# Performance work log

Hardware: AMD Instinct MI355X
Metric: run time of the kernel (lower is better)

## Reference

```python
import jax, jax.numpy as jnp
import numpy as np

EMBED = 1024
HEADS = 16
HEAD_DIM = EMBED // HEADS


def setup_inputs() -> dict:
    key = jax.random.key(0)
    k1, k2, k3, k4, k5 = jax.random.split(key, 5)
    B, S, E = 4, 2048, EMBED
    scale = 1.0 / np.sqrt(E)
    return {
        "tensor": jax.random.normal(k1, (B, S, E), dtype=jnp.float32),
        "in_proj_w": jax.random.normal(k2, (3 * E, E), dtype=jnp.float32) * scale,
        "in_proj_b": jax.random.normal(k3, (3 * E,), dtype=jnp.float32) * 0.02,
        "out_proj_w": jax.random.normal(k4, (E, E), dtype=jnp.float32) * scale,
        "out_proj_b": jax.random.normal(k5, (E,), dtype=jnp.float32) * 0.02,
        "causal_mask": 1,
    }


def reference(tensor, in_proj_w, in_proj_b, out_proj_w, out_proj_b, causal_mask):
    B, S, E = tensor.shape
    H, D = HEADS, HEAD_DIM
    # fused qkv projection (torch Linear: x @ W.T + b)
    qkv = tensor @ in_proj_w.T + in_proj_b  # [B, S, 3E]
    q, k, v = jnp.split(qkv, 3, axis=-1)
    # [B, S, E] -> [B, H, S, D]
    q = q.reshape(B, S, H, D).transpose(0, 2, 1, 3)
    k = k.reshape(B, S, H, D).transpose(0, 2, 1, 3)
    v = v.reshape(B, S, H, D).transpose(0, 2, 1, 3)
    scores = jnp.einsum("bhqd,bhkd->bhqk", q, k)  # [B, H, S, S]
    if causal_mask:
        mask = jnp.triu(jnp.ones((S, S), dtype=bool), k=1)
        scores = jnp.where(mask, -jnp.inf, scores)
    scores = scores / np.sqrt(D).astype(np.float32)
    attn = jax.nn.softmax(scores, axis=-1)
    out = jnp.einsum("bhqk,bhkd->bhqd", attn, v)  # [B, H, S, D]
    out = out.transpose(0, 2, 1, 3).reshape(B, S, E)
    return out @ out_proj_w.T + out_proj_b
```

## Files before the change

### kernel.cpp

```cpp
#include <hip/hip_runtime.h>
#include <hip/hip_bf16.h>

#define B_  4
#define S_  2048
#define E_  1024
#define H_  16
#define D_  64
#define M_  (B_*S_)
#define N3_ (3*E_)

typedef __bf16 bf16;
typedef bf16  bf16x4 __attribute__((ext_vector_type(4)));
typedef bf16  bf16x8 __attribute__((ext_vector_type(8)));
typedef float f32x4  __attribute__((ext_vector_type(4)));

#define SC2 0.18033688011112043f

__device__ __forceinline__ f32x4 mfma16(bf16x8 a, bf16x8 b, f32x4 c) {
    return __builtin_amdgcn_mfma_f32_16x16x32_bf16(a, b, c, 0, 0, 0);
}

typedef const __attribute__((address_space(1))) void* gas_t;
typedef __attribute__((address_space(3))) void* las_t;
__device__ __forceinline__ void gl_lds16(const void* g, void* l) {
    __builtin_amdgcn_global_load_lds((gas_t)g, (las_t)l, 16, 0, 0);
}

#define WAITCNT_VM4() __builtin_amdgcn_s_waitcnt(0x0F74)
#define WAITCNT_VM2() __builtin_amdgcn_s_waitcnt(0x0F72)
#define WAITCNT_VM0() __builtin_amdgcn_s_waitcnt(0x0F70)

__global__ __launch_bounds__(256) void cvt_all(const float* __restrict__ x,
                                               const float* __restrict__ w_in,
                                               const float* __restrict__ w_out,
                                               bf16* __restrict__ Xbf,
                                               bf16* __restrict__ Wqkv,
                                               bf16* __restrict__ Wo) {
    const int n1 = M_ * E_ / 4, n2 = N3_ * E_ / 4, n3 = E_ * E_ / 4;
    int i = blockIdx.x * blockDim.x + threadIdx.x;
    const float* src; bf16* dst; int j;
    if (i < n1)           { src = x;     dst = Xbf;  j = i; }
    else if (i < n1 + n2) { src = w_in;  dst = Wqkv; j = i - n1; }
    else if (i < n1 + n2 + n3) { src = w_out; dst = Wo; j = i - n1 - n2; }
    else return;
    float4 v = *(const float4*)(src + (size_t)j * 4);
    bf16x4 o;
    o[0] = (bf16)v.x; o[1] = (bf16)v.y; o[2] = (bf16)v.z; o[3] = (bf16)v.w;
    *(bf16x4*)(dst + (size_t)j * 4) = o;
}

__global__ __launch_bounds__(256) void gemm_qkv(const bf16* __restrict__ X,
                                                const bf16* __restrict__ W,
                                                const float* __restrict__ bias,
                                                bf16* __restrict__ QKV,
                                                bf16* __restrict__ Vt) {
    __shared__ __align__(16) bf16 As[128 * 64];
    __shared__ __align__(16) bf16 Bs[128 * 64];
    const int t = threadIdx.x;
    const int wav = t >> 6, lane = t & 63, quad = lane >> 4, l15 = lane & 15;
    const int m0 = blockIdx.y * 128, n0 = blockIdx.x * 128;
    const int wr = (wav >> 1) * 64, wc = (wav & 1) * 64;
    const int srow = t >> 3;
    const int swz  = ((t & 7) ^ (srow & 7)) * 8;
    const bool isV = (n0 >= 2 * E_);

    const bf16* Ablk = X + (size_t)m0 * E_;
    const bf16* Bblk = W + (size_t)n0 * E_;
    f32x4 acc[4][4] = {};

    for (int kk = 0; kk < E_; kk += 64) {
        __syncthreads();
        #pragma unroll
        for (int ps = 0; ps < 4; ++ps) {
            gl_lds16(Ablk + (size_t)(srow + ps * 32) * E_ + kk + swz, As + (size_t)(t + ps * 256) * 8);
            gl_lds16(Bblk + (size_t)(srow + ps * 32) * E_ + kk + swz, Bs + (size_t)(t + ps * 256) * 8);
        }
        __syncthreads();
        #pragma unroll
        for (int ks = 0; ks < 2; ++ks) {
            bf16x8 af[4], bw[4];
            #pragma unroll
            for (int i = 0; i < 4; ++i) {
                const int ra = wr + i * 16 + l15;
                const int rb = wc + i * 16 + l15;
                const int cx = ((ks * 4 + quad) ^ (l15 & 7)) * 8;
                af[i] = *(const bf16x8*)&As[ra * 64 + cx];
                bw[i] = *(const bf16x8*)&Bs[rb * 64 + cx];
            }
            if (!isV) {
                #pragma unroll
                for (int i = 0; i < 4; ++i)
                    #pragma unroll
                    for (int j = 0; j < 4; ++j)
                        acc[i][j] = mfma16(af[i], bw[j], acc[i][j]);
            } else {
                #pragma unroll
                for (int i = 0; i < 4; ++i)
                    #pragma unroll
                    for (int j = 0; j < 4; ++j)
                        acc[i][j] = mfma16(bw[i], af[j], acc[i][j]);
            }
        }
    }
    if (!isV) {
        #pragma unroll
        for (int i = 0; i < 4; ++i)
            #pragma unroll
            for (int j = 0; j < 4; ++j)
                #pragma unroll
                for (int r = 0; r < 4; ++r) {
                    int mg = m0 + wr + i * 16 + quad * 4 + r;
                    int ng = n0 + wc + j * 16 + l15;
                    float v = acc[i][j][r] + bias[ng];
                    int which = ng >> 10, rem = ng & 1023;
                    if (which == 0) v *= SC2;
                    int h = rem >> 6, d = rem & 63;
                    int b = mg >> 11, s = mg & 2047;
                    QKV[(size_t)which * (B_ * H_ * S_ * D_) +
                        (((size_t)(b * H_ + h) * S_ + s) * D_ + d)] = (bf16)v;
                }
    } else {
        #pragma unroll
        for (int i = 0; i < 4; ++i)
            #pragma unroll
            for (int j = 0; j < 4; ++j)
                #pragma unroll
                for (int r = 0; r < 4; ++r) {
                    int ng = n0 + wc + i * 16 + quad * 4 + r;
                    int mg = m0 + wr + j * 16 + l15;
                    float v = acc[i][j][r] + bias[ng];
                    int rem = ng & 1023;
                    int h = rem >> 6, d = rem & 63;
                    int b = mg >> 11, s = mg & 2047;
                    Vt[(((size_t)(b * H_ + h) * D_ + d) * S_) + s] = (bf16)v;
                }
    }
}

__global__ __launch_bounds__(512, 4) void attn8(const bf16* __restrict__ Q,
                                                const bf16* __restrict__ K,
                                                const bf16* __restrict__ Vt,
                                                bf16* __restrict__ O) {
    __shared__ __align__(16) bf16 Ks[2][64 * 64];
    __shared__ __align__(16) bf16 Vs[2][64 * 64];
    __shared__ __align__(16) bf16 Ps[8][16 * 64];

    const int t = threadIdx.x;
    const int wav = t >> 6, lane = t & 63, quad = lane >> 4, l15 = lane & 15;
    const int p  = blockIdx.x >> 6;
    const int bh = blockIdx.x & 63;

    const bf16* Qb = Q  + (size_t)bh * S_ * D_;
    const bf16* Kb = K  + (size_t)bh * S_ * D_;
    const bf16* Vb = Vt + (size_t)bh * (size_t)D_ * S_;

    const int srow = t >> 3;
    const int swz  = ((t & 7) ^ (srow & 7)) * 8;
    bf16* Pw = &Ps[wav][0];
    const int pswz = l15 & 7;

    const int b = bh >> 4, h = bh & 15;

    #pragma unroll 1
    for (int phase = 0; phase < 2; ++phase) {
        const int qb  = phase ? (15 - p) : p;
        const int q0w = qb * 128 + wav * 16;
        const int qg  = q0w + l15;
        const int niter = 2 * qb + 2;

        __builtin_amdgcn_s_barrier();
        gl_lds16(Kb + (size_t)srow * D_ + swz, &Ks[0][(size_t)t * 8]);
        gl_lds16(Vb + (size_t)srow * S_ + swz, &Vs[0][(size_t)t * 8]);

        bf16x8 qf0 = *(const bf16x8*)&Qb[(size_t)(q0w + l15) * D_ + quad * 8];
        bf16x8 qf1 = *(const bf16x8*)&Qb[(size_t)(q0w + l15) * D_ + 32 + quad * 8];

        f32x4 oacc[4] = {};
        f32x4 psum = {0.f, 0.f, 0.f, 0.f};

        #pragma unroll 1
        for (int it = 0; it < niter; ++it) {
            const int key0 = it * 64;
            const int cur = it & 1;
            const bf16* Kc = &Ks[cur][0];
            const bf16* Vc = &Vs[cur][0];

            __builtin_amdgcn_s_barrier();
            if (it + 1 < niter) {
                const int kn = key0 + 64;
                gl_lds16(Kb + (size_t)(kn + srow) * D_ + swz, &Ks[1 - cur][(size_t)t * 8]);
                gl_lds16(Vb + (size_t)srow * S_ + kn + swz,   &Vs[1 - cur][(size_t)t * 8]);
                WAITCNT_VM2();
            } else {
                WAITCNT_VM0();
            }
            __builtin_amdgcn_s_barrier();

            f32x4 sacc[4];
            #pragma unroll
            for (int mt = 0; mt < 4; ++mt) {
                const int krow = mt * 16 + l15;
                const int sw = krow & 7;
                bf16x8 kf0 = *(const bf16x8*)&Kc[krow * 64 + ((quad ^ sw) * 8)];
                bf16x8 kf1 = *(const bf16x8*)&Kc[krow * 64 + (((4 + quad) ^ sw) * 8)];
                f32x4 a = {};
                a = mfma16(kf0, qf0, a);
                a = mfma16(kf1, qf1, a);
                sacc[mt] = a;
            }

            #pragma unroll
            for (int mt = 0; mt < 4; ++mt) {
                if (key0 + mt * 16 + 15 > q0w) {
                    #pragma unroll
                    for (int r = 0; r < 4; ++r) {
                        int key = key0 + mt * 16 + quad * 4 + r;
                        sacc[mt][r] = (key > qg) ? -3e38f : sacc[mt][r];
                    }
                }
            }

            #pragma unroll
            for (int mt = 0; mt < 4; ++mt) {
                bf16x4 pk;
                #pragma unroll
                for (int r = 0; r < 4; ++r) {
                    float pv = __builtin_amdgcn_exp2f(sacc[mt][r]);
                    psum[r] += pv;
                    pk[r] = (bf16)pv;
                }
                const int pc = ((mt * 2 + (quad >> 1)) ^ pswz) * 8 + (quad & 1) * 4;
                *(bf16x4*)&Pw[l15 * 64 + pc] = pk;
            }

            bf16x8 pf0 = *(const bf16x8*)&Pw[l15 * 64 + ((quad ^ pswz) * 8)];
            bf16x8 pf1 = *(const bf16x8*)&Pw[l15 * 64 + (((4 + quad) ^ pswz) * 8)];
            #pragma unroll
            for (int nt = 0; nt < 4; ++nt) {
                const int vrow = nt * 16 + l15;
                const int sw = vrow & 7;
                bf16x8 vf0 = *(const bf16x8*)&Vc[vrow * 64 + ((quad ^ sw) * 8)];
                bf16x8 vf1 = *(const bf16x8*)&Vc[vrow * 64 + (((4 + quad) ^ sw) * 8)];
                oacc[nt] = mfma16(pf0, vf0, oacc[nt]);
                oacc[nt] = mfma16(pf1, vf1, oacc[nt]);
            }
        }

        float rsum = psum[0] + psum[1] + psum[2] + psum[3];
        rsum += __shfl_xor(rsum, 16);
        rsum += __shfl_xor(rsum, 32);
        const float linv = 1.0f / rsum;

        #pragma unroll
        for (int rr = 0; rr < 4; ++rr) {
            float li = __shfl(linv, quad * 4 + rr);
            const int q = q0w + quad * 4 + rr;
            #pragma unroll
            for (int nt = 0; nt < 4; ++nt)
                O[((size_t)b * S_ + q) * E_ + h * D_ + nt * 16 + l15] =
                    (bf16)(oacc[nt][rr] * li);
        }
    }
}

__global__ __launch_bounds__(256) void gemm_out(const bf16* __restrict__ A,
                                                const bf16* __restrict__ W,
                                                const float* __restrict__ bias,
                                                float* __restrict__ out) {
    __shared__ __align__(16) bf16 As[128 * 64];
    __shared__ __align__(16) bf16 Bs[128 * 64];
    const int t = threadIdx.x;
    const int wav = t >> 6, lane = t & 63, quad = lane >> 4, l15 = lane & 15;
    const int m0 = blockIdx.y * 128, n0 = blockIdx.x * 128;
    const int wr = (wav >> 1) * 64, wc = (wav & 1) * 64;
    const int srow = t >> 3;
    const int swz  = ((t & 7) ^ (srow & 7)) * 8;

    const bf16* Ablk = A + (size_t)m0 * E_;
    const bf16* Bblk = W + (size_t)n0 * E_;
    f32x4 acc[4][4] = {};

    for (int kk = 0; kk < E_; kk += 64) {
        __syncthreads();
        #pragma unroll
        for (int ps = 0; ps < 4; ++ps) {
            gl_lds16(Ablk + (size_t)(srow + ps * 32) * E_ + kk + swz, As + (size_t)(t + ps * 256) * 8);
            gl_lds16(Bblk + (size_t)(srow + ps * 32) * E_ + kk + swz, Bs + (size_t)(t + ps * 256) * 8);
        }
        __syncthreads();
        #pragma unroll
        for (int ks = 0; ks < 2; ++ks) {
            bf16x8 af[4], bw[4];
            #pragma unroll
            for (int i = 0; i < 4; ++i) {
                const int ra = wr + i * 16 + l15;
                const int rb = wc + i * 16 + l15;
                const int cx = ((ks * 4 + quad) ^ (l15 & 7)) * 8;
                af[i] = *(const bf16x8*)&As[ra * 64 + cx];
                bw[i] = *(const bf16x8*)&Bs[rb * 64 + cx];
            }
            #pragma unroll
            for (int i = 0; i < 4; ++i)
                #pragma unroll
                for (int j = 0; j < 4; ++j)
                    acc[i][j] = mfma16(af[i], bw[j], acc[i][j]);
        }
    }
    #pragma unroll
    for (int i = 0; i < 4; ++i)
        #pragma unroll
        for (int j = 0; j < 4; ++j)
            #pragma unroll
            for (int r = 0; r < 4; ++r) {
                int mg = m0 + wr + i * 16 + quad * 4 + r;
                int ng = n0 + wc + j * 16 + l15;
                out[(size_t)mg * E_ + ng] = acc[i][j][r] + bias[ng];
            }
}

extern "C" void kernel_launch(void* const* d_in, const int* in_sizes, int n_in,
                              void* d_out, int out_size, void* d_ws, size_t ws_size,
                              hipStream_t stream) {
    const float* x     = (const float*)d_in[0];
    const float* w_in  = (const float*)d_in[1];
    const float* b_in  = (const float*)d_in[2];
    const float* w_out = (const float*)d_in[3];
    const float* b_out = (const float*)d_in[4];
    float* out = (float*)d_out;

    char* ws = (char*)d_ws;
    bf16* Xbf  = (bf16*)ws; ws += (size_t)M_ * E_ * 2;
    bf16* Wqkv = (bf16*)ws; ws += (size_t)N3_ * E_ * 2;
    bf16* Wo   = (bf16*)ws; ws += (size_t)E_ * E_ * 2;
    bf16* QKV  = (bf16*)ws; ws += (size_t)2 * B_ * H_ * S_ * D_ * 2;
    bf16* Vt   = (bf16*)ws; ws += (size_t)B_ * H_ * S_ * D_ * 2;
    bf16* Obf  = Xbf;

    const int nCvt = (M_ * E_ + N3_ * E_ + E_ * E_) / 4;
    cvt_all<<<(nCvt + 255) / 256, 256, 0, stream>>>(x, w_in, w_out, Xbf, Wqkv, Wo);

    gemm_qkv<<<dim3(N3_ / 128, M_ / 128), 256, 0, stream>>>(Xbf, Wqkv, b_in, QKV, Vt);

    bf16* Qp = QKV;
    bf16* Kp = QKV + (size_t)B_ * H_ * S_ * D_;

    attn8<<<dim3(8 * B_ * H_), 512, 0, stream>>>(Qp, Kp, Vt, Obf);

    gemm_out<<<dim3(E_ / 128, M_ / 128), 256, 0, stream>>>(Obf, Wo, b_out, out);
}
```

Before: 233.5 us.

## Double attention key/value tile size to 128 keys per iteration

The attention kernel now stages 128 keys of K and V per LDS buffer instead of 64, halving the loop iterations and barrier pairs per query block. Inside each iteration it processes two 64-key sub-tiles and skips the second when it lies fully above the causal diagonal. V uses a 128-wide row with a 16-way XOR swizzle. LDS use grows from about 48 KB to about 80 KB per block, which may lower the number of resident blocks per CU. The wasted masked work on the diagonal tile also grows.

```diff
diff --git a/kernel.cpp b/kernel.cpp
--- a/kernel.cpp
+++ b/kernel.cpp
@@ -27,7 +27,6 @@
 }
 
 #define WAITCNT_VM4() __builtin_amdgcn_s_waitcnt(0x0F74)
-#define WAITCNT_VM2() __builtin_amdgcn_s_waitcnt(0x0F72)
 #define WAITCNT_VM0() __builtin_amdgcn_s_waitcnt(0x0F70)
 
 __global__ __launch_bounds__(256) void cvt_all(const float* __restrict__ x,
@@ -137,12 +136,12 @@
     }
 }
 
-__global__ __launch_bounds__(512, 4) void attn8(const bf16* __restrict__ Q,
+__global__ __launch_bounds__(512, 4) void attn9(const bf16* __restrict__ Q,
                                                 const bf16* __restrict__ K,
                                                 const bf16* __restrict__ Vt,
                                                 bf16* __restrict__ O) {
-    __shared__ __align__(16) bf16 Ks[2][64 * 64];
-    __shared__ __align__(16) bf16 Vs[2][64 * 64];
+    __shared__ __align__(16) bf16 Ks[2][128 * 64];
+    __shared__ __align__(16) bf16 Vs[2][64 * 128];
     __shared__ __align__(16) bf16 Ps[8][16 * 64];
 
     const int t = threadIdx.x;
@@ -156,6 +155,9 @@
 
     const int srow = t >> 3;
     const int swz  = ((t & 7) ^ (srow & 7)) * 8;
+    const int vrow_st = t >> 4;
+    const int vswz = ((t & 15) ^ (vrow_st & 15)) * 8;
+
     bf16* Pw = &Ps[wav][0];
     const int pswz = l15 & 7;
 
@@ -166,11 +168,13 @@
         const int qb  = phase ? (15 - p) : p;
         const int q0w = qb * 128 + wav * 16;
         const int qg  = q0w + l15;
-        const int niter = 2 * qb + 2;
+        const int niter = qb + 1;
 
         __builtin_amdgcn_s_barrier();
-        gl_lds16(Kb + (size_t)srow * D_ + swz, &Ks[0][(size_t)t * 8]);
-        gl_lds16(Vb + (size_t)srow * S_ + swz, &Vs[0][(size_t)t * 8]);
+        gl_lds16(Kb + (size_t)srow * D_ + swz,            &Ks[0][(size_t)t * 8]);
+        gl_lds16(Kb + (size_t)(srow + 64) * D_ + swz,     &Ks[0][(size_t)(t + 512) * 8]);
+        gl_lds16(Vb + (size_t)vrow_st * S_ + vswz,        &Vs[0][(size_t)t * 8]);
+        gl_lds16(Vb + (size_t)(vrow_st + 32) * S_ + vswz, &Vs[0][(size_t)(t + 512) * 8]);
 
         bf16x8 qf0 = *(const bf16x8*)&Qb[(size_t)(q0w + l15) * D_ + quad * 8];
         bf16x8 qf1 = *(const bf16x8*)&Qb[(size_t)(q0w + l15) * D_ + 32 + quad * 8];
@@ -180,69 +184,79 @@
 
         #pragma unroll 1
         for (int it = 0; it < niter; ++it) {
-            const int key0 = it * 64;
+            const int key0 = it * 128;
             const int cur = it & 1;
             const bf16* Kc = &Ks[cur][0];
             const bf16* Vc = &Vs[cur][0];
 
             __builtin_amdgcn_s_barrier();
             if (it + 1 < niter) {
-                const int kn = key0 + 64;
-                gl_lds16(Kb + (size_t)(kn + srow) * D_ + swz, &Ks[1 - cur][(size_t)t * 8]);
-                gl_lds16(Vb + (size_t)srow * S_ + kn + swz,   &Vs[1 - cur][(size_t)t * 8]);
-                WAITCNT_VM2();
+                const int kn = key0 + 128;
+                bf16* Kn = &Ks[1 - cur][0];
+                bf16* Vn = &Vs[1 - cur][0];
+                gl_lds16(Kb + (size_t)(kn + srow) * D_ + swz,        Kn + (size_t)t * 8);
+                gl_lds16(Kb + (size_t)(kn + srow + 64) * D_ + swz,   Kn + (size_t)(t + 512) * 8);
+                gl_lds16(Vb + (size_t)vrow_st * S_ + kn + vswz,        Vn + (size_t)t * 8);
+                gl_lds16(Vb + (size_t)(vrow_st + 32) * S_ + kn + vswz, Vn + (size_t)(t + 512) * 8);
+                WAITCNT_VM4();
             } else {
                 WAITCNT_VM0();
             }
             __builtin_amdgcn_s_barrier();
 
-            f32x4 sacc[4];
-            #pragma unroll
-            for (int mt = 0; mt < 4; ++mt) {
-                const int krow = mt * 16 + l15;
-                const int sw = krow & 7;
-                bf16x8 kf0 = *(const bf16x8*)&Kc[krow * 64 + ((quad ^ sw) * 8)];
-                bf16x8 kf1 = *(const bf16x8*)&Kc[krow * 64 + (((4 + quad) ^ sw) * 8)];
-                f32x4 a = {};
-                a = mfma16(kf0, qf0, a);
-                a = mfma16(kf1, qf1, a);
-                sacc[mt] = a;
-            }
-
-            #pragma unroll
-            for (int mt = 0; mt < 4; ++mt) {
-                if (key0 + mt * 16 + 15 > q0w) {
+            #pragma unroll
+            for (int sub = 0; sub < 2; ++sub) {
+                const int key0s = key0 + sub * 64;
+                if (sub == 1 && q0w + 15 < key0s) continue;
+
+                f32x4 sacc[4];
+                #pragma unroll
+                for (int mt = 0; mt < 4; ++mt) {
+                    const int krow = sub * 64 + mt * 16 + l15;
+                    const int sw = krow & 7;
+                    bf16x8 kf0 = *(const bf16x8*)&Kc[krow * 64 + ((quad ^ sw) * 8)];
+                    bf16x8 kf1 = *(const bf16x8*)&Kc[krow * 64 + (((4 + quad) ^ sw) * 8)];
+                    f32x4 a = {};
+                    a = mfma16(kf0, qf0, a);
+                    a = mfma16(kf1, qf1, a);
+                    sacc[mt] = a;
+                }
+
+                #pragma unroll
+                for (int mt = 0; mt < 4; ++mt) {
+                    if (key0s + mt * 16 + 15 > q0w) {
+                        #pragma unroll
+                        for (int r = 0; r < 4; ++r) {
+                            int key = key0s + mt * 16 + quad * 4 + r;
+                            sacc[mt][r] = (key > qg) ? -3e38f : sacc[mt][r];
+                        }
+                    }
+                }
+
+                #pragma unroll
+                for (int mt = 0; mt < 4; ++mt) {
+                    bf16x4 pk;
                     #pragma unroll
                     for (int r = 0; r < 4; ++r) {
-                        int key = key0 + mt * 16 + quad * 4 + r;
-                        sacc[mt][r] = (key > qg) ? -3e38f : sacc[mt][r];
+                        float pv = __builtin_amdgcn_exp2f(sacc[mt][r]);
+                        psum[r] += pv;
+                        pk[r] = (bf16)pv;
                     }
-                }
-            }
-
-            #pragma unroll
-            for (int mt = 0; mt < 4; ++mt) {
-                bf16x4 pk;
-                #pragma unroll
-                for (int r = 0; r < 4; ++r) {
-                    float pv = __builtin_amdgcn_exp2f(sacc[mt][r]);
-                    psum[r] += pv;
-                    pk[r] = (bf16)pv;
-                }
-                const int pc = ((mt * 2 + (quad >> 1)) ^ pswz) * 8 + (quad & 1) * 4;
-                *(bf16x4*)&Pw[l15 * 64 + pc] = pk;
-            }
-
-            bf16x8 pf0 = *(const bf16x8*)&Pw[l15 * 64 + ((quad ^ pswz) * 8)];
-            bf16x8 pf1 = *(const bf16x8*)&Pw[l15 * 64 + (((4 + quad) ^ pswz) * 8)];
-            #pragma unroll
-            for (int nt = 0; nt < 4; ++nt) {
-                const int vrow = nt * 16 + l15;
-                const int sw = vrow & 7;
-                bf16x8 vf0 = *(const bf16x8*)&Vc[vrow * 64 + ((quad ^ sw) * 8)];
-                bf16x8 vf1 = *(const bf16x8*)&Vc[vrow * 64 + (((4 + quad) ^ sw) * 8)];
-                oacc[nt] = mfma16(pf0, vf0, oacc[nt]);
-                oacc[nt] = mfma16(pf1, vf1, oacc[nt]);
+                    const int pc = ((mt * 2 + (quad >> 1)) ^ pswz) * 8 + (quad & 1) * 4;
+                    *(bf16x4*)&Pw[l15 * 64 + pc] = pk;
+                }
+
+                bf16x8 pf0 = *(const bf16x8*)&Pw[l15 * 64 + ((quad ^ pswz) * 8)];
+                bf16x8 pf1 = *(const bf16x8*)&Pw[l15 * 64 + (((4 + quad) ^ pswz) * 8)];
+                #pragma unroll
+                for (int nt = 0; nt < 4; ++nt) {
+                    const int vrow = nt * 16 + l15;
+                    const int sw16 = vrow & 15;
+                    bf16x8 vf0 = *(const bf16x8*)&Vc[vrow * 128 + (((sub * 8 + quad) ^ sw16) * 8)];
+                    bf16x8 vf1 = *(const bf16x8*)&Vc[vrow * 128 + (((sub * 8 + 4 + quad) ^ sw16) * 8)];
+                    oacc[nt] = mfma16(pf0, vf0, oacc[nt]);
+                    oacc[nt] = mfma16(pf1, vf1, oacc[nt]);
+                }
             }
         }
 
@@ -344,7 +358,7 @@
     bf16* Qp = QKV;
     bf16* Kp = QKV + (size_t)B_ * H_ * S_ * D_;
 
-    attn8<<<dim3(8 * B_ * H_), 512, 0, stream>>>(Qp, Kp, Vt, Obf);
+    attn9<<<dim3(8 * B_ * H_), 512, 0, stream>>>(Qp, Kp, Vt, Obf);
 
     gemm_out<<<dim3(E_ / 128, M_ / 128), 256, 0, stream>>>(Obf, Wo, b_out, out);
 }
```

New measurement: 235.8 us. Within noise of the previous version (+1.0%).
